# Optimization experiments

Measured on AMD Instinct MI355X. Metric: run time of the kernel, lower is better.

## Reference

```python
import jax, jax.numpy as jnp
import numpy as np

EMBED = 512
HEADS = 8
FMUL = 4
TAU = 2.0
V_TH = 1.0      # spiking threshold (spikingjelly default)
ALPHA = 2.0     # ATan surrogate alpha (spikingjelly default)
EPS = 1e-5


@jax.custom_vjp
def spike_fn(v):
    # Heaviside spike with ATan surrogate gradient (spikingjelly surrogate.ATan)
    return (v >= V_TH).astype(v.dtype)

def _spike_fwd(v):
    return spike_fn(v), v

def _spike_bwd(v, g):
    t = (jnp.pi / 2.0) * ALPHA * (v - V_TH)
    return (g * (ALPHA / 2.0) / (1.0 + t * t),)

spike_fn.defvjp(_spike_fwd, _spike_bwd)


def layernorm(x, g, b):
    mu = jnp.mean(x, axis=-1, keepdims=True)
    var = jnp.mean(jnp.square(x - mu), axis=-1, keepdims=True)
    return (x - mu) * jax.lax.rsqrt(var + EPS) * g + b


def setup_inputs() -> dict:
    key = jax.random.key(0)
    ks = jax.random.split(key, 12)
    m, s, e = 4, 2048, EMBED
    f = e * FMUL
    sc = 0.02
    return {
        "x":  jax.random.normal(ks[0], (m, s, e), jnp.float32),
        "wq": jax.random.normal(ks[1], (e, e), jnp.float32) * sc,
        "bq": jnp.zeros((e,), jnp.float32),
        "wk": jax.random.normal(ks[2], (e, e), jnp.float32) * sc,
        "bk": jnp.zeros((e,), jnp.float32),
        "wv": jax.random.normal(ks[3], (e, e), jnp.float32) * sc,
        "bv": jnp.zeros((e,), jnp.float32),
        "w1": jax.random.normal(ks[4], (e, f), jnp.float32) * sc,
        "b1": jnp.zeros((f,), jnp.float32),
        "w2": jax.random.normal(ks[5], (f, e), jnp.float32) * sc,
        "b2": jnp.zeros((e,), jnp.float32),
        "g1": jnp.ones((e,), jnp.float32),
        "be1": jnp.zeros((e,), jnp.float32),
        "g2": jnp.ones((e,), jnp.float32),
        "be2": jnp.zeros((e,), jnp.float32),
    }


def reference(x, wq, bq, wk, bk, wv, bv, w1, b1, w2, b2, g1, be1, g2, be2):
    m, s, e = x.shape
    h = HEADS
    d = e // h

    # --- pre-norm attention (NOTE: original has NO 1/sqrt(d) scaling) ---
    n1 = layernorm(x, g1, be1)
    q = (n1 @ wq + bq).reshape(m, s, h, d).transpose(0, 2, 1, 3)  # [m,h,s,d]
    k = (n1 @ wk + bk).reshape(m, s, h, d).transpose(0, 2, 1, 3)
    v = (n1 @ wv + bv).reshape(m, s, h, d).transpose(0, 2, 1, 3)
    scores = jnp.einsum('bhqd,bhkd->bhqk', q, k)       # [m,h,s,s], unscaled
    attn = jax.nn.softmax(scores, axis=-1)
    ctx = jnp.einsum('bhqk,bhkd->bhqd', attn, v)       # [m,h,s,d]
    att_out = ctx.transpose(0, 2, 1, 3).reshape(m, s, e)

    x = x + att_out
    # dropout p=0.4 is identity at inference (eval path in the original)

    # --- FFN with spiking activation ---
    n2 = layernorm(x, g2, be2)
    h1 = n2 @ w1 + b1                                  # [m,s,4e]
    # single-step LIF charge from v=0: v = v + (x - v)/tau = x/tau
    spikes = spike_fn(h1 / TAU)
    return x + (spikes @ w2 + b2)
```

## Files before the change

### kernel.cpp

```cpp
#include <hip/hip_runtime.h>
#include <stdint.h>

#define EMB 512
#define SEQ 2048
#define MB 4
#define NH 8
#define HD 64
#define ROWS (MB*SEQ)
#define MARGIN 0.02f
#define CAP 65536
#define LOG2E 1.44269504f
#define EXPB (-17.3123405f)

typedef unsigned short u16;
typedef __attribute__((ext_vector_type(8))) short bf16x8;
typedef __attribute__((ext_vector_type(4))) float f32x4;
typedef __attribute__((ext_vector_type(2))) unsigned int u32x2;
typedef __attribute__((ext_vector_type(4))) unsigned int u32x4;

union Frag { u32x2 u[2]; bf16x8 v; };
union Frag4 { unsigned u[4]; bf16x8 v; };

__device__ __forceinline__ u16 f2bf(float f) {
  union { float f; unsigned u; } a; a.f = f;
  unsigned r = a.u + 0x7FFFu + ((a.u >> 16) & 1u);
  return (u16)(r >> 16);
}
__device__ __forceinline__ float bflo(unsigned u) {
  union { unsigned u; float f; } c; c.u = u << 16; return c.f;
}
__device__ __forceinline__ float bfhi(unsigned u) {
  union { unsigned u; float f; } c; c.u = u & 0xffff0000u; return c.f;
}
__device__ __forceinline__ void gld16(const void* g, void* l) {
  __builtin_amdgcn_global_load_lds(
      (const __attribute__((address_space(1))) void*)g,
      (__attribute__((address_space(3))) void*)l, 16, 0, 0);
}


__global__ __launch_bounds__(256) void k_prep(
    const float* __restrict__ x, const float* __restrict__ g1, const float* __restrict__ be1,
    const float* __restrict__ wq, const float* __restrict__ wk,
    const float* __restrict__ wv, const float* __restrict__ w1,
    u16* __restrict__ n1, u16* __restrict__ wqkvT, u16* __restrict__ w1T,
    int* __restrict__ cnt) {
  __shared__ float tile[32][33];
  int b = blockIdx.x, tid = threadIdx.x;
  if (b < 1792) {
    const float* src; u16* dst; int N, bx, by;
    if (b < 768) {
      int z = b >> 8, rem = b & 255; bx = rem & 15; by = rem >> 4; N = 512;
      src = (z == 0) ? wq : ((z == 1) ? wk : wv);
      dst = wqkvT + z * 512 * 512;
    } else {
      int rem = b - 768; bx = rem & 63; by = rem >> 6; N = 2048;
      src = w1; dst = w1T;
    }
    int tx = tid & 31, ty = tid >> 5;
    int k0 = by * 32, n0 = bx * 32;
    for (int i = 0; i < 32; i += 8)
      tile[ty + i][tx] = src[(size_t)(k0 + ty + i) * N + n0 + tx];
    __syncthreads();
    for (int i = 0; i < 32; i += 8)
      dst[(size_t)(n0 + ty + i) * 512 + k0 + tx] = f2bf(tile[tx][ty + i]);
  } else {
    if (b == 1792 && tid < 2) cnt[tid] = 0;
    int wid = tid >> 6, lane = tid & 63;
    int row = (b - 1792) * 4 + wid;
    const float* xr = x + (size_t)row * EMB + lane * 8;
    f32x4 v0 = *(const f32x4*)xr;
    f32x4 v1 = *(const f32x4*)(xr + 4);
    float s = v0.x+v0.y+v0.z+v0.w + v1.x+v1.y+v1.z+v1.w;
    float q = v0.x*v0.x+v0.y*v0.y+v0.z*v0.z+v0.w*v0.w
            + v1.x*v1.x+v1.y*v1.y+v1.z*v1.z+v1.w*v1.w;
    #pragma unroll
    for (int o = 1; o < 64; o <<= 1) { s += __shfl_xor(s, o); q += __shfl_xor(q, o); }
    float mu = s * (1.0f/512.0f);
    float rs = 1.0f / sqrtf(q * (1.0f/512.0f) - mu*mu + 1e-5f);
    f32x4 ga = *(const f32x4*)(g1 + lane*8), gb = *(const f32x4*)(g1 + lane*8 + 4);
    f32x4 ba = *(const f32x4*)(be1 + lane*8), bb = *(const f32x4*)(be1 + lane*8 + 4);
    union { u16 h[8]; u32x4 v; } o8;
    o8.h[0] = f2bf((v0.x-mu)*rs*ga.x + ba.x); o8.h[1] = f2bf((v0.y-mu)*rs*ga.y + ba.y);
    o8.h[2] = f2bf((v0.z-mu)*rs*ga.z + ba.z); o8.h[3] = f2bf((v0.w-mu)*rs*ga.w + ba.w);
    o8.h[4] = f2bf((v1.x-mu)*rs*gb.x + bb.x); o8.h[5] = f2bf((v1.y-mu)*rs*gb.y + bb.y);
    o8.h[6] = f2bf((v1.z-mu)*rs*gb.z + bb.z); o8.h[7] = f2bf((v1.w-mu)*rs*gb.w + bb.w);
    *(u32x4*)(n1 + (size_t)row * EMB + lane * 8) = o8.v;
  }
}

__global__ __launch_bounds__(256) void k_ln2(const float* __restrict__ x,
    const u16* __restrict__ att, const float* __restrict__ g, const float* __restrict__ b,
    const float* __restrict__ b2, float* __restrict__ x2, u16* __restrict__ n2,
    float* __restrict__ out) {
  int wid = threadIdx.x >> 6, lane = threadIdx.x & 63;
  int row = blockIdx.x * 4 + wid;
  size_t base = (size_t)row * EMB + lane * 8;
  u32x4 av = *(const u32x4*)(att + base);
  f32x4 t0, t1;
  t0.x = bflo(av.x); t0.y = bfhi(av.x); t0.z = bflo(av.y); t0.w = bfhi(av.y);
  t1.x = bflo(av.z); t1.y = bfhi(av.z); t1.z = bflo(av.w); t1.w = bfhi(av.w);
  f32x4 v0 = *(const f32x4*)(x + base)     + t0;
  f32x4 v1 = *(const f32x4*)(x + base + 4) + t1;
  *(f32x4*)(x2 + base) = v0;
  *(f32x4*)(x2 + base + 4) = v1;
  *(f32x4*)(out + base)     = v0 + *(const f32x4*)(b2 + lane*8);
  *(f32x4*)(out + base + 4) = v1 + *(const f32x4*)(b2 + lane*8 + 4);
  float s = v0.x+v0.y+v0.z+v0.w + v1.x+v1.y+v1.z+v1.w;
  float q = v0.x*v0.x+v0.y*v0.y+v0.z*v0.z+v0.w*v0.w
          + v1.x*v1.x+v1.y*v1.y+v1.z*v1.z+v1.w*v1.w;
  #pragma unroll
  for (int o = 1; o < 64; o <<= 1) { s += __shfl_xor(s, o); q += __shfl_xor(q, o); }
  float mu = s * (1.0f/512.0f);
  float rs = 1.0f / sqrtf(q * (1.0f/512.0f) - mu*mu + 1e-5f);
  f32x4 ga = *(const f32x4*)(g + lane*8), gb = *(const f32x4*)(g + lane*8 + 4);
  f32x4 ba = *(const f32x4*)(b + lane*8), bb = *(const f32x4*)(b + lane*8 + 4);
  union { u16 h[8]; u32x4 v; } o8;
  o8.h[0] = f2bf((v0.x-mu)*rs*ga.x + ba.x); o8.h[1] = f2bf((v0.y-mu)*rs*ga.y + ba.y);
  o8.h[2] = f2bf((v0.z-mu)*rs*ga.z + ba.z); o8.h[3] = f2bf((v0.w-mu)*rs*ga.w + ba.w);
  o8.h[4] = f2bf((v1.x-mu)*rs*gb.x + bb.x); o8.h[5] = f2bf((v1.y-mu)*rs*gb.y + bb.y);
  o8.h[6] = f2bf((v1.z-mu)*rs*gb.z + bb.z); o8.h[7] = f2bf((v1.w-mu)*rs*gb.w + bb.w);
  *(u32x4*)(n2 + (size_t)row * EMB + lane * 8) = o8.v;
}

#define GEMM_CORE(A_, Bt_, m0_, n0_)                                           \
  __shared__ u16 As[2][128 * 32];                                              \
  __shared__ u16 Bs[2][128 * 32];                                              \
  int tid = threadIdx.x;                                                       \
  int wid = tid >> 6, lane = tid & 63;                                         \
  int quad = lane >> 4, ln15 = lane & 15;                                      \
  int wm = (wid >> 1) * 64, wn = (wid & 1) * 64;                               \
  int arow = lane >> 2, acol = (lane & 3) * 8;                                 \
  const u16* gA0 = A_  + (size_t)(m0_ + wid * 32 + arow) * 512 + acol;         \
  const u16* gA1 = gA0 + (size_t)16 * 512;                                     \
  const u16* gB0 = Bt_ + (size_t)(n0_ + wid * 32 + arow) * 512 + acol;         \
  const u16* gB1 = gB0 + (size_t)16 * 512;                                     \
  f32x4 acc[4][4] = {};                                                        \
  gld16(gA0, &As[0][(wid * 32) * 32]); gld16(gA1, &As[0][(wid * 32 + 16) * 32]);\
  gld16(gB0, &Bs[0][(wid * 32) * 32]); gld16(gB1, &Bs[0][(wid * 32 + 16) * 32]);\
  for (int kt = 0; kt < 16; kt++) {                                            \
    int cur = kt & 1;                                                          \
    __syncthreads();                                                           \
    if (kt < 15) {                                                             \
      int ko = (kt + 1) * 32;                                                  \
      gld16(gA0 + ko, &As[cur ^ 1][(wid * 32) * 32]);                          \
      gld16(gA1 + ko, &As[cur ^ 1][(wid * 32 + 16) * 32]);                     \
      gld16(gB0 + ko, &Bs[cur ^ 1][(wid * 32) * 32]);                          \
      gld16(gB1 + ko, &Bs[cur ^ 1][(wid * 32 + 16) * 32]);                     \
    }                                                                          \
    bf16x8 af[4], bf[4];                                                       \
    _Pragma("unroll")                                                          \
    for (int i = 0; i < 4; i++) {                                              \
      af[i] = *(const bf16x8*)&As[cur][(wm + i * 16 + ln15) * 32 + quad * 8];  \
      bf[i] = *(const bf16x8*)&Bs[cur][(wn + i * 16 + ln15) * 32 + quad * 8];  \
    }                                                                          \
    _Pragma("unroll")                                                          \
    for (int i = 0; i < 4; i++)                                                \
      _Pragma("unroll")                                                        \
      for (int j = 0; j < 4; j++)                                              \
        acc[i][j] = __builtin_amdgcn_mfma_f32_16x16x32_bf16(af[i], bf[j],      \
                                                            acc[i][j], 0, 0, 0);\
  }                                                                            \
  __syncthreads();

__global__ __launch_bounds__(256) void k_gemm_qkv(
    const u16* __restrict__ A, const u16* __restrict__ Bt,
    const float* __restrict__ bq, const float* __restrict__ bk, const float* __restrict__ bv,
    u16* __restrict__ Qb, u16* __restrict__ Kb, u16* __restrict__ Vtb) {
  int m0 = blockIdx.y * 128, n0 = blockIdx.x * 128;
  GEMM_CORE(A, Bt, m0, n0)
  #pragma unroll
  for (int j = 0; j < 4; j++) {
    int n = n0 + wn + j * 16 + ln15;
    int t = n >> 9, cc = n & 511, head = cc >> 6, dd = cc & 63;
    float bias = (t == 0) ? bq[cc] : ((t == 1) ? bk[cc] : bv[cc]);
    #pragma unroll
    for (int i = 0; i < 4; i++) {
      int row0 = m0 + wm + i * 16 + quad * 4;
      int mm = row0 >> 11, ss0 = row0 & 2047;
      if (t == 2) {
        union { u16 h[4]; u32x2 v; } pk;
        #pragma unroll
        for (int r = 0; r < 4; r++) pk.h[r] = f2bf(acc[i][j][r] + bias);
        *(u32x2*)(Vtb + ((size_t)(mm * 8 + head) * 64 + dd) * 2048 + ss0) = pk.v;
      } else {
        u16* dst = (t == 0) ? Qb : Kb;
        #pragma unroll
        for (int r = 0; r < 4; r++)
          dst[((size_t)(mm * 8 + head) * 2048 + ss0 + r) * 64 + dd] =
              f2bf(acc[i][j][r] + bias);
      }
    }
  }
}

__global__ __launch_bounds__(256) void k_gemm_ffn1(
    const u16* __restrict__ A, const u16* __restrict__ Bt, const float* __restrict__ b1,
    int* __restrict__ cnt, unsigned* __restrict__ spikeL, unsigned* __restrict__ candL) {
  int m0 = blockIdx.y * 128, n0 = blockIdx.x * 128;
  GEMM_CORE(A, Bt, m0, n0)
  #pragma unroll
  for (int j = 0; j < 4; j++) {
    int n = n0 + wn + j * 16 + ln15;
    float bias = b1[n];
    #pragma unroll
    for (int i = 0; i < 4; i++) {
      #pragma unroll
      for (int r = 0; r < 4; r++) {
        int row = m0 + wm + i * 16 + quad * 4 + r;
        float hv = acc[i][j][r] + bias;
        if (hv >= 2.0f - MARGIN) {
          if (hv >= 2.0f + MARGIN) {
            int ix = atomicAdd(&cnt[0], 1);
            if (ix < CAP) spikeL[ix] = (unsigned)(row * 2048 + n);
          } else {
            int ix = atomicAdd(&cnt[1], 1);
            if (ix < CAP) candL[ix] = (unsigned)(row * 2048 + n);
          }
        }
      }
    }
  }
}

#define F_STAGE(BUF, T0)                                                       \
  do {                                                                         \
    gld16(gK0 + (size_t)(T0) * 4096, &L.SB[BUF][0][(rb +  0) * 64]);           \
    gld16(gK1 + (size_t)(T0) * 4096, &L.SB[BUF][0][(rb +  8) * 64]);           \
    gld16(gK2 + (size_t)(T0) * 4096, &L.SB[BUF][0][(rb + 16) * 64]);           \
    gld16(gK3 + (size_t)(T0) * 4096, &L.SB[BUF][0][(rb + 24) * 64]);           \
    gld16(gV0 + (T0) * 64, &L.SB[BUF][1][(rb +  0) * 64]);                     \
    gld16(gV1 + (T0) * 64, &L.SB[BUF][1][(rb +  8) * 64]);                     \
    gld16(gV2 + (T0) * 64, &L.SB[BUF][1][(rb + 16) * 64]);                     \
    gld16(gV3 + (T0) * 64, &L.SB[BUF][1][(rb + 24) * 64]);                     \
  } while (0)

#define F_INNER(BUF)                                                           \
  do {                                                                         \
    const u16* Kc = L.SB[BUF][0];                                              \
    const u16* Vc = L.SB[BUF][1];                                              \
    f32x4 s4[2][4];                                                            \
    __builtin_amdgcn_s_setprio(1);                                             \
    _Pragma("unroll")                                                          \
    for (int j = 0; j < 4; j++) {                                              \
      bf16x8 a = *(const bf16x8*)(Kc + (j * 16 + ln15) * 64 + ((quad ^ lm) * 8)); \
      s4[0][j] = __builtin_amdgcn_mfma_f32_16x16x32_bf16(a, aQ[0][0].v, z4, 0, 0, 0); \
      s4[1][j] = __builtin_amdgcn_mfma_f32_16x16x32_bf16(a, aQ[1][0].v, z4, 0, 0, 0); \
    }                                                                          \
    _Pragma("unroll")                                                          \
    for (int j = 0; j < 4; j++) {                                              \
      bf16x8 a = *(const bf16x8*)(Kc + (j * 16 + ln15) * 64 + (((4 + quad) ^ lm) * 8)); \
      s4[0][j] = __builtin_amdgcn_mfma_f32_16x16x32_bf16(a, aQ[0][1].v, s4[0][j], 0, 0, 0); \
      s4[1][j] = __builtin_amdgcn_mfma_f32_16x16x32_bf16(a, aQ[1][1].v, s4[1][j], 0, 0, 0); \
    }                                                                          \
    __builtin_amdgcn_s_setprio(0);                                             \
    Frag4 bP[2][2];                                                            \
    _Pragma("unroll")                                                          \
    for (int h = 0; h < 2; h++) {                                              \
      unsigned pr[4][4];                                                       \
      _Pragma("unroll")                                                        \
      for (int j = 0; j < 4; j++)                                              \
        _Pragma("unroll")                                                      \
        for (int r = 0; r < 4; r++) {                                          \
          float p = __builtin_amdgcn_exp2f(fmaf(s4[h][j][r], LOG2E, EXPB));    \
          l4[h][r] += p;                                                       \
          union { float f; unsigned u; } cc; cc.f = p;                         \
          pr[j][r] = cc.u;                                                     \
        }                                                                      \
      _Pragma("unroll")                                                        \
      for (int t = 0; t < 2; t++) {                                            \
        bP[h][t].u[0] = __builtin_amdgcn_perm(pr[2*t][1],   pr[2*t][0],   0x07060302u); \
        bP[h][t].u[1] = __builtin_amdgcn_perm(pr[2*t][3],   pr[2*t][2],   0x07060302u); \
        bP[h][t].u[2] = __builtin_amdgcn_perm(pr[2*t+1][1], pr[2*t+1][0], 0x07060302u); \
        bP[h][t].u[3] = __builtin_amdgcn_perm(pr[2*t+1][3], pr[2*t+1][2], 0x07060302u); \
      }                                                                        \
    }                                                                          \
    __builtin_amdgcn_s_setprio(1);                                             \
    _Pragma("unroll")                                                          \
    for (int t = 0; t < 2; t++)                                                \
      _Pragma("unroll")                                                        \
      for (int j = 0; j < 4; j++) {                                            \
        int row = j * 16 + ln15;                                               \
        int c0 = 4 * t + (quad >> 1), sub = (quad & 1) * 4;                    \
        Frag aV;                                                               \
        aV.u[0] = *(const u32x2*)(Vc + row * 64 + ((c0 ^ lm) * 8) + sub);      \
        aV.u[1] = *(const u32x2*)(Vc + row * 64 + (((c0 + 2) ^ lm) * 8) + sub);\
        U[0][j] = __builtin_amdgcn_mfma_f32_16x16x32_bf16(aV.v, bP[0][t].v,    \
                                                          U[0][j], 0, 0, 0);   \
        U[1][j] = __builtin_amdgcn_mfma_f32_16x16x32_bf16(aV.v, bP[1][t].v,    \
                                                          U[1][j], 0, 0, 0);   \
      }                                                                        \
    __builtin_amdgcn_s_setprio(0);                                             \
  } while (0)

__global__ __launch_bounds__(128, 4) void k_flash(
    const u16* __restrict__ Q, const u16* __restrict__ K,
    const u16* __restrict__ Vt, u16* __restrict__ att) {
  __shared__ union {
    u16 SB[2][2][64 * 64];
    float T[2][16 * 68];
  } L;
  int tid = threadIdx.x, wid = tid >> 6, lane = tid & 63;
  int quad = lane >> 4, ln15 = lane & 15, lm = ln15 & 7;
  int qb = blockIdx.x, head = blockIdx.y, mm = blockIdx.z;
  int mh = mm * 8 + head;
  const u16* Qp = Q  + (size_t)mh * SEQ * HD;
  const u16* Kp = K  + (size_t)mh * SEQ * HD;
  const u16* Vp = Vt + (size_t)mh * HD * SEQ;
  int q0 = qb * 64 + wid * 32;

  Frag aQ[2][2];
  #pragma unroll
  for (int h = 0; h < 2; h++)
    #pragma unroll
    for (int t = 0; t < 2; t++) {
      u32x4 g = *(const u32x4*)(Qp + (size_t)(q0 + h * 16 + ln15) * 64 + t * 32 + quad * 8);
      aQ[h][t].u[0].x = g.x; aQ[h][t].u[0].y = g.y;
      aQ[h][t].u[1].x = g.z; aQ[h][t].u[1].y = g.w;
    }
  const f32x4 z4 = {0.f, 0.f, 0.f, 0.f};

  int srow = lane >> 3;
  int sch  = (lane & 7) ^ (srow & 7);
  int rb = wid * 32;
  const u16* gK0 = Kp + (size_t)(rb +  0 + srow) * 64 + sch * 8;
  const u16* gK1 = Kp + (size_t)(rb +  8 + srow) * 64 + sch * 8;
  const u16* gK2 = Kp + (size_t)(rb + 16 + srow) * 64 + sch * 8;
  const u16* gK3 = Kp + (size_t)(rb + 24 + srow) * 64 + sch * 8;
  const u16* gV0 = Vp + (size_t)(rb +  0 + srow) * SEQ + sch * 8;
  const u16* gV1 = Vp + (size_t)(rb +  8 + srow) * SEQ + sch * 8;
  const u16* gV2 = Vp + (size_t)(rb + 16 + srow) * SEQ + sch * 8;
  const u16* gV3 = Vp + (size_t)(rb + 24 + srow) * SEQ + sch * 8;

  f32x4 l4[2] = {{0.f,0.f,0.f,0.f}, {0.f,0.f,0.f,0.f}};
  f32x4 U[2][4] = {};

  F_STAGE(0, 0);
  for (int it = 0; it < 16; it++) {
    __syncthreads();
    F_STAGE(1, 2 * it + 1);
    F_INNER(0);
    __syncthreads();
    if (it < 15) F_STAGE(0, 2 * it + 2);
    F_INNER(1);
  }
  __syncthreads();

  #pragma unroll
  for (int h = 0; h < 2; h++) {
    float lv = l4[h].x + l4[h].y + l4[h].z + l4[h].w;
    lv += __shfl_xor(lv, 16);
    lv += __shfl_xor(lv, 32);
    float rl = 1.0f / lv;
    float* Tw = L.T[wid];
    #pragma unroll
    for (int j = 0; j < 4; j++)
      *(f32x4*)(Tw + ln15 * 68 + j * 16 + quad * 4) = U[h][j] * rl;
    #pragma unroll
    for (int s = 0; s < 4; s++) {
      f32x4 o = *(const f32x4*)(Tw + (quad * 4 + s) * 68 + ln15 * 4);
      union { u16 h4[4]; u32x2 v; } pk;
      pk.h4[0] = f2bf(o.x); pk.h4[1] = f2bf(o.y);
      pk.h4[2] = f2bf(o.z); pk.h4[3] = f2bf(o.w);
      *(u32x2*)(att + ((size_t)mm * SEQ + q0 + h * 16 + quad * 4 + s) * EMB +
                head * 64 + ln15 * 4) = pk.v;
    }
  }
}

__global__ __launch_bounds__(256) void k_fixup(
    const float* __restrict__ x2, const float* __restrict__ w1, const float* __restrict__ b1,
    const float* __restrict__ g2, const float* __restrict__ be2,
    int* __restrict__ cnt, unsigned* __restrict__ spikeL, const unsigned* __restrict__ candL) {
  __shared__ float sb[8];
  int tid = threadIdx.x;
  int nC = cnt[1]; if (nC > CAP) nC = CAP;
  for (int e = blockIdx.x; e < nC; e += gridDim.x) {
    unsigned v = candL[e];
    int row = (int)(v >> 11), col = (int)(v & 2047u);
    const float* xr = x2 + (size_t)row * 512;
    float x0 = xr[tid], x1 = xr[tid + 256];
    float s = x0 + x1, q = x0 * x0 + x1 * x1;
    #pragma unroll
    for (int o = 1; o < 64; o <<= 1) { s += __shfl_xor(s, o); q += __shfl_xor(q, o); }
    if ((tid & 63) == 0) { sb[tid >> 6] = s; sb[4 + (tid >> 6)] = q; }
    __syncthreads();
    float st = sb[0] + sb[1] + sb[2] + sb[3];
    float qt = sb[4] + sb[5] + sb[6] + sb[7];
    __syncthreads();
    float mu = st * (1.f / 512.f);
    float rs = 1.f / sqrtf(qt * (1.f / 512.f) - mu * mu + 1e-5f);
    float na = (x0 - mu) * rs * g2[tid] + be2[tid];
    float nb = (x1 - mu) * rs * g2[tid + 256] + be2[tid + 256];
    float dd = na * w1[(size_t)tid * 2048 + col] + nb * w1[(size_t)(tid + 256) * 2048 + col];
    #pragma unroll
    for (int o = 1; o < 64; o <<= 1) dd += __shfl_xor(dd, o);
    if ((tid & 63) == 0) sb[tid >> 6] = dd;
    __syncthreads();
    if (tid == 0) {
      float hv = sb[0] + sb[1] + sb[2] + sb[3] + b1[col];
      if (hv >= 2.0f) { int ix = atomicAdd(&cnt[0], 1); if (ix < CAP) spikeL[ix] = v; }
    }
    __syncthreads();
  }
}

__global__ void k_apply(const float* __restrict__ w2, const int* __restrict__ cnt,
                        const unsigned* __restrict__ spikeL, float* __restrict__ out) {
  int n = cnt[0]; if (n > CAP) n = CAP;
  int tid = threadIdx.x;
  for (int e = blockIdx.x; e < n; e += gridDim.x) {
    unsigned v = spikeL[e];
    int row = (int)(v >> 11), col = (int)(v & 2047u);
    atomicAdd(&out[(size_t)row * 512 + tid * 2 + 0], w2[(size_t)col * 512 + tid * 2 + 0]);
    atomicAdd(&out[(size_t)row * 512 + tid * 2 + 1], w2[(size_t)col * 512 + tid * 2 + 1]);
  }
}


extern "C" void kernel_launch(void* const* d_in, const int* in_sizes, int n_in,
                              void* d_out, int out_size, void* d_ws, size_t ws_size,
                              hipStream_t stream) {
  (void)in_sizes; (void)n_in; (void)out_size; (void)ws_size;
  const float* x   = (const float*)d_in[0];
  const float* wq  = (const float*)d_in[1];
  const float* bq  = (const float*)d_in[2];
  const float* wk  = (const float*)d_in[3];
  const float* bk  = (const float*)d_in[4];
  const float* wv  = (const float*)d_in[5];
  const float* bv  = (const float*)d_in[6];
  const float* w1  = (const float*)d_in[7];
  const float* b1  = (const float*)d_in[8];
  const float* w2  = (const float*)d_in[9];
  const float* b2  = (const float*)d_in[10];
  const float* g1  = (const float*)d_in[11];
  const float* be1 = (const float*)d_in[12];
  const float* g2  = (const float*)d_in[13];
  const float* be2 = (const float*)d_in[14];
  float* out = (float*)d_out;

  char* w = (char*)d_ws;
  size_t off = 0;
  auto take = [&](size_t bytes) { char* p = w + off; off += (bytes + 255) & ~(size_t)255; return p; };
  int*      cnt    = (int*)take(256);
  u16*      n1     = (u16*)take((size_t)ROWS * EMB * 2);
  u16*      wqkvT  = (u16*)take((size_t)1536 * 512 * 2);
  u16*      w1T    = (u16*)take((size_t)2048 * 512 * 2);
  u16*      Qb     = (u16*)take((size_t)MB * NH * SEQ * HD * 2);
  u16*      Kb     = (u16*)take((size_t)MB * NH * SEQ * HD * 2);
  u16*      Vtb    = (u16*)take((size_t)MB * NH * SEQ * HD * 2);
  u16*      att    = (u16*)take((size_t)ROWS * EMB * 2);
  float*    x2     = (float*)take((size_t)ROWS * EMB * 4);
  u16*      n2     = (u16*)take((size_t)ROWS * EMB * 2);
  unsigned* spikeL = (unsigned*)take((size_t)CAP * 4);
  unsigned* candL  = (unsigned*)take((size_t)CAP * 4);

  k_prep<<<3840, 256, 0, stream>>>(x, g1, be1, wq, wk, wv, w1, n1, wqkvT, w1T, cnt);
  k_gemm_qkv<<<dim3(12, 64), 256, 0, stream>>>(n1, wqkvT, bq, bk, bv, Qb, Kb, Vtb);
  k_flash<<<dim3(32, 8, 4), 128, 0, stream>>>(Qb, Kb, Vtb, att);
  k_ln2<<<ROWS / 4, 256, 0, stream>>>(x, att, g2, be2, b2, x2, n2, out);
  k_gemm_ffn1<<<dim3(16, 64), 256, 0, stream>>>(n2, w1T, b1, cnt, spikeL, candL);
  k_fixup<<<256, 256, 0, stream>>>(x2, w1, b1, g2, be2, cnt, spikeL, candL);
  k_apply<<<128, 256, 0, stream>>>(w2, cnt, spikeL, out);
}
```

Before: 218.0 us.

## Double per-wave query rows in flash attention and compute row sums via MFMA

Each wave now handles 64 query rows instead of 32, so every K/V tile staged in shared memory is reused across twice as many queries and the grid halves. The softmax denominator is now accumulated with an extra MFMA against a bf16 ones fragment instead of scalar adds plus cross-lane shuffles, and it sums the bf16-rounded probabilities. Block indices are swizzled to spread heads and batches across the grid. The cost is higher register pressure, with launch bounds lowered to 2 blocks per SM, and fewer blocks (512) to fill the GPU.

```diff
diff --git a/kernel.cpp b/kernel.cpp
--- a/kernel.cpp
+++ b/kernel.cpp
@@ -239,31 +239,32 @@
   do {                                                                         \
     const u16* Kc = L.SB[BUF][0];                                              \
     const u16* Vc = L.SB[BUF][1];                                              \
-    f32x4 s4[2][4];                                                            \
+    f32x4 s4[4][4];                                                            \
     __builtin_amdgcn_s_setprio(1);                                             \
     _Pragma("unroll")                                                          \
     for (int j = 0; j < 4; j++) {                                              \
       bf16x8 a = *(const bf16x8*)(Kc + (j * 16 + ln15) * 64 + ((quad ^ lm) * 8)); \
-      s4[0][j] = __builtin_amdgcn_mfma_f32_16x16x32_bf16(a, aQ[0][0].v, z4, 0, 0, 0); \
-      s4[1][j] = __builtin_amdgcn_mfma_f32_16x16x32_bf16(a, aQ[1][0].v, z4, 0, 0, 0); \
+      _Pragma("unroll")                                                        \
+      for (int h = 0; h < 4; h++)                                              \
+        s4[h][j] = __builtin_amdgcn_mfma_f32_16x16x32_bf16(a, aQ[h][0].v, z4, 0, 0, 0); \
     }                                                                          \
     _Pragma("unroll")                                                          \
     for (int j = 0; j < 4; j++) {                                              \
       bf16x8 a = *(const bf16x8*)(Kc + (j * 16 + ln15) * 64 + (((4 + quad) ^ lm) * 8)); \
-      s4[0][j] = __builtin_amdgcn_mfma_f32_16x16x32_bf16(a, aQ[0][1].v, s4[0][j], 0, 0, 0); \
-      s4[1][j] = __builtin_amdgcn_mfma_f32_16x16x32_bf16(a, aQ[1][1].v, s4[1][j], 0, 0, 0); \
+      _Pragma("unroll")                                                        \
+      for (int h = 0; h < 4; h++)                                              \
+        s4[h][j] = __builtin_amdgcn_mfma_f32_16x16x32_bf16(a, aQ[h][1].v, s4[h][j], 0, 0, 0); \
     }                                                                          \
     __builtin_amdgcn_s_setprio(0);                                             \
-    Frag4 bP[2][2];                                                            \
-    _Pragma("unroll")                                                          \
-    for (int h = 0; h < 2; h++) {                                              \
+    Frag4 bP[4][2];                                                            \
+    _Pragma("unroll")                                                          \
+    for (int h = 0; h < 4; h++) {                                              \
       unsigned pr[4][4];                                                       \
       _Pragma("unroll")                                                        \
       for (int j = 0; j < 4; j++)                                              \
         _Pragma("unroll")                                                      \
         for (int r = 0; r < 4; r++) {                                          \
           float p = __builtin_amdgcn_exp2f(fmaf(s4[h][j][r], LOG2E, EXPB));    \
-          l4[h][r] += p;                                                       \
           union { float f; unsigned u; } cc; cc.f = p;                         \
           pr[j][r] = cc.u;                                                     \
         }                                                                      \
@@ -279,21 +280,27 @@
     _Pragma("unroll")                                                          \
     for (int t = 0; t < 2; t++)                                                \
       _Pragma("unroll")                                                        \
+      for (int h = 0; h < 4; h++)                                              \
+        lacc[h] = __builtin_amdgcn_mfma_f32_16x16x32_bf16(vOne.v, bP[h][t].v,  \
+                                                          lacc[h], 0, 0, 0);   \
+    _Pragma("unroll")                                                          \
+    for (int t = 0; t < 2; t++)                                                \
+      _Pragma("unroll")                                                        \
       for (int j = 0; j < 4; j++) {                                            \
         int row = j * 16 + ln15;                                               \
         int c0 = 4 * t + (quad >> 1), sub = (quad & 1) * 4;                    \
         Frag aV;                                                               \
         aV.u[0] = *(const u32x2*)(Vc + row * 64 + ((c0 ^ lm) * 8) + sub);      \
         aV.u[1] = *(const u32x2*)(Vc + row * 64 + (((c0 + 2) ^ lm) * 8) + sub);\
-        U[0][j] = __builtin_amdgcn_mfma_f32_16x16x32_bf16(aV.v, bP[0][t].v,    \
-                                                          U[0][j], 0, 0, 0);   \
-        U[1][j] = __builtin_amdgcn_mfma_f32_16x16x32_bf16(aV.v, bP[1][t].v,    \
-                                                          U[1][j], 0, 0, 0);   \
+        _Pragma("unroll")                                                      \
+        for (int h = 0; h < 4; h++)                                            \
+          U[h][j] = __builtin_amdgcn_mfma_f32_16x16x32_bf16(aV.v, bP[h][t].v,  \
+                                                            U[h][j], 0, 0, 0); \
       }                                                                        \
     __builtin_amdgcn_s_setprio(0);                                             \
   } while (0)
 
-__global__ __launch_bounds__(128, 4) void k_flash(
+__global__ __launch_bounds__(128, 2) void k_flash(
     const u16* __restrict__ Q, const u16* __restrict__ K,
     const u16* __restrict__ Vt, u16* __restrict__ att) {
   __shared__ union {
@@ -302,16 +309,18 @@
   } L;
   int tid = threadIdx.x, wid = tid >> 6, lane = tid & 63;
   int quad = lane >> 4, ln15 = lane & 15, lm = ln15 & 7;
-  int qb = blockIdx.x, head = blockIdx.y, mm = blockIdx.z;
+  int bid = blockIdx.x + 16 * (blockIdx.y + 8 * (int)blockIdx.z);
+  int swz = (bid & 7) * 64 + (bid >> 3);
+  int qb = swz & 15, head = (swz >> 4) & 7, mm = swz >> 7;
   int mh = mm * 8 + head;
   const u16* Qp = Q  + (size_t)mh * SEQ * HD;
   const u16* Kp = K  + (size_t)mh * SEQ * HD;
   const u16* Vp = Vt + (size_t)mh * HD * SEQ;
-  int q0 = qb * 64 + wid * 32;
-
-  Frag aQ[2][2];
+  int q0 = qb * 128 + wid * 64;
+
+  Frag aQ[4][2];
   #pragma unroll
-  for (int h = 0; h < 2; h++)
+  for (int h = 0; h < 4; h++)
     #pragma unroll
     for (int t = 0; t < 2; t++) {
       u32x4 g = *(const u32x4*)(Qp + (size_t)(q0 + h * 16 + ln15) * 64 + t * 32 + quad * 8);
@@ -319,6 +328,9 @@
       aQ[h][t].u[1].x = g.z; aQ[h][t].u[1].y = g.w;
     }
   const f32x4 z4 = {0.f, 0.f, 0.f, 0.f};
+  Frag4 vOne;
+  vOne.u[0] = 0x3F803F80u; vOne.u[1] = 0x3F803F80u;
+  vOne.u[2] = 0x3F803F80u; vOne.u[3] = 0x3F803F80u;
 
   int srow = lane >> 3;
   int sch  = (lane & 7) ^ (srow & 7);
@@ -332,8 +344,8 @@
   const u16* gV2 = Vp + (size_t)(rb + 16 + srow) * SEQ + sch * 8;
   const u16* gV3 = Vp + (size_t)(rb + 24 + srow) * SEQ + sch * 8;
 
-  f32x4 l4[2] = {{0.f,0.f,0.f,0.f}, {0.f,0.f,0.f,0.f}};
-  f32x4 U[2][4] = {};
+  f32x4 lacc[4] = {};
+  f32x4 U[4][4] = {};
 
   F_STAGE(0, 0);
   for (int it = 0; it < 16; it++) {
@@ -347,11 +359,8 @@
   __syncthreads();
 
   #pragma unroll
-  for (int h = 0; h < 2; h++) {
-    float lv = l4[h].x + l4[h].y + l4[h].z + l4[h].w;
-    lv += __shfl_xor(lv, 16);
-    lv += __shfl_xor(lv, 32);
-    float rl = 1.0f / lv;
+  for (int h = 0; h < 4; h++) {
+    float rl = 1.0f / lacc[h][0];
     float* Tw = L.T[wid];
     #pragma unroll
     for (int j = 0; j < 4; j++)
@@ -457,7 +466,7 @@
 
   k_prep<<<3840, 256, 0, stream>>>(x, g1, be1, wq, wk, wv, w1, n1, wqkvT, w1T, cnt);
   k_gemm_qkv<<<dim3(12, 64), 256, 0, stream>>>(n1, wqkvT, bq, bk, bv, Qb, Kb, Vtb);
-  k_flash<<<dim3(32, 8, 4), 128, 0, stream>>>(Qb, Kb, Vtb, att);
+  k_flash<<<dim3(16, 8, 4), 128, 0, stream>>>(Qb, Kb, Vtb, att);
   k_ln2<<<ROWS / 4, 256, 0, stream>>>(x, att, g2, be2, b2, x2, n2, out);
   k_gemm_ffn1<<<dim3(16, 64), 256, 0, stream>>>(n2, w1T, b1, cnt, spikeL, candL);
   k_fixup<<<256, 256, 0, stream>>>(x2, w1, b1, g2, be2, cnt, spikeL, candL);
```

After: 229.0 us. 5.0% more time.
